# Kernel tuning notes

Measured on AMD Instinct MI355X. Metric: run time of the kernel, lower is better.

## Reference

```python
import jax, jax.numpy as jnp
import numpy as np


def setup_inputs() -> dict:
    key = jax.random.key(0)
    k1, k2, k3 = jax.random.split(key, 3)
    B, F, H, W = 16, 16, 256, 256
    inp = jax.random.normal(k1, (B, F, H, W), dtype=jnp.float32)
    target = jax.random.normal(k2, (B, F, H, W), dtype=jnp.float32)
    masks = jax.random.randint(k3, (B, F, H, W), 0, 2).astype(jnp.bool_)
    hull = jnp.zeros((1,), dtype=jnp.int32)  # unused by the module's forward
    return {"input": inp, "target": target, "masks": masks, "hull": hull}


def _masked_mean_per_feature(diff, w):
    # diff: [B,F,H,W]; w: float mask broadcastable to diff. Returns [F] masked means
    # with 0.0 where the mask is empty (matching the torch `if len(diff) > 0` guard).
    s = jnp.sum(diff * w, axis=(0, 2, 3))                               # [F]
    c = jnp.sum(jnp.broadcast_to(w, diff.shape), axis=(0, 2, 3))        # [F]
    return jnp.where(c > 0, s / jnp.maximum(c, 1.0), 0.0)


def reference(input, target, masks, hull):
    diff = jnp.abs(input - target)                                      # [B,F,H,W]
    m = masks.astype(diff.dtype)                                        # feature masks
    m_not = 1.0 - m                                                     # background
    m_all = jnp.any(masks, axis=1, keepdims=True).astype(diff.dtype)    # [B,1,H,W]

    loss_features = jnp.mean(_masked_mean_per_feature(diff, m))
    loss_background = jnp.mean(_masked_mean_per_feature(diff, m_not))
    loss_all_features = jnp.mean(_masked_mean_per_feature(diff, m_all))

    return (loss_features + loss_all_features + loss_background) / 3.0
```

## Files before the change

kernel.cpp:

```cpp
#include <hip/hip_runtime.h>

constexpr int B = 16, F = 16, H = 256, W = 256;
constexpr int HW = H * W;
constexpr int SPATIAL = B * HW;
constexpr int PLANE4 = HW / 4;
constexpr int BSTRIDE4 = F * PLANE4;
constexpr int FQ = 4;

constexpr int NBLK = 2048;
constexpr int NTHREADS = 256;
constexpr int NWAVES = NTHREADS / 64;
constexpr int TOTG = B * PLANE4;
constexpr int SLOTS = NBLK * NWAVES * 16;
constexpr int G = TOTG / SLOTS;
static_assert(G == 2, "kernel below is hand-scheduled for G==2");

constexpr int NVALS = 50;

struct Buf {
    unsigned int m[FQ];
    float4 a[FQ];
    float4 t[FQ];
};

__global__ __launch_bounds__(NTHREADS) void heatloss_main(
        const float4* __restrict__ inp, const float4* __restrict__ tgt,
        const unsigned int* __restrict__ msk, float* __restrict__ partials) {
    const int tid  = threadIdx.x;
    const int wave = tid >> 6;
    const int lane = tid & 63;
    const int l16  = lane & 15;
    const int q    = lane >> 4;
    const int slot0 = (blockIdx.x * NWAVES + wave) * 16 + l16;
    const int qoff  = q * (FQ * PLANE4);

    float s[FQ]  = {0.f, 0.f, 0.f, 0.f};
    float c[FQ]  = {0.f, 0.f, 0.f, 0.f};
    float dt[FQ] = {0.f, 0.f, 0.f, 0.f};
    float sall = 0.f, call = 0.f;

    auto load_group = [&](Buf& bf, int it) {
        const int slot = slot0 + it * SLOTS;
        const int base = (slot >> 14) * BSTRIDE4 + (slot & (PLANE4 - 1)) + qoff;
        #pragma unroll
        for (int j = 0; j < FQ; j++) bf.m[j] = msk[base + j * PLANE4];
        #pragma unroll
        for (int j = 0; j < FQ; j++) bf.a[j] = inp[base + j * PLANE4];
        #pragma unroll
        for (int j = 0; j < FQ; j++) bf.t[j] = tgt[base + j * PLANE4];
    };

    auto consume = [&](const Buf& bf) {
        unsigned int anyu = bf.m[0] | bf.m[1] | bf.m[2] | bf.m[3];
        anyu |= __shfl_xor(anyu, 16, 64);
        anyu |= __shfl_xor(anyu, 32, 64);
        const float af0 = (anyu & 0x000000FFu) ? 1.f : 0.f;
        const float af1 = (anyu & 0x0000FF00u) ? 1.f : 0.f;
        const float af2 = (anyu & 0x00FF0000u) ? 1.f : 0.f;
        const float af3 = (anyu & 0xFF000000u) ? 1.f : 0.f;
        if (q == 0) call += (af0 + af1) + (af2 + af3);

        #pragma unroll
        for (int j = 0; j < FQ; j++) {
            const float4 a = bf.a[j];
            const float4 t = bf.t[j];
            const float d0 = fabsf(a.x - t.x);
            const float d1 = fabsf(a.y - t.y);
            const float d2 = fabsf(a.z - t.z);
            const float d3 = fabsf(a.w - t.w);
            const unsigned int mm = bf.m[j];
            const float m0 = (float)( mm        & 0xFFu);
            const float m1 = (float)((mm >> 8)  & 0xFFu);
            const float m2 = (float)((mm >> 16) & 0xFFu);
            const float m3 = (float)( mm >> 24);
            dt[j] += (d0 + d1) + (d2 + d3);
            s[j]  += m0 * d0 + m1 * d1 + m2 * d2 + m3 * d3;
            c[j]  += (m0 + m1) + (m2 + m3);
            sall  += af0 * d0 + af1 * d1 + af2 * d2 + af3 * d3;
        }
    };

    Buf b0, b1;
    load_group(b0, 0);
    load_group(b1, 1);
    asm volatile("" ::: "memory");
    consume(b0);
    consume(b1);

    __shared__ float red[NWAVES][NVALS];
    const int fbase = q * FQ;
    #pragma unroll
    for (int j = 0; j < FQ; j++) {
        float xs = s[j], xc = c[j], xd = dt[j];
        #pragma unroll
        for (int o = 8; o > 0; o >>= 1) {
            xs += __shfl_down(xs, o, 16);
            xc += __shfl_down(xc, o, 16);
            xd += __shfl_down(xd, o, 16);
        }
        if (l16 == 0) {
            red[wave][ 0 + fbase + j] = xs;
            red[wave][16 + fbase + j] = xc;
            red[wave][32 + fbase + j] = xd;
        }
    }
    float xa = sall, xcl = call;
    #pragma unroll
    for (int o = 32; o > 0; o >>= 1) {
        xa  += __shfl_down(xa,  o, 64);
        xcl += __shfl_down(xcl, o, 64);
    }
    if (lane == 0) { red[wave][48] = xa; red[wave][49] = xcl; }
    __syncthreads();

    if (tid < NVALS) {
        float t = 0.f;
        #pragma unroll
        for (int w2 = 0; w2 < NWAVES; w2++) t += red[w2][tid];
        partials[tid * NBLK + blockIdx.x] = t;
    }
}

__global__ __launch_bounds__(NTHREADS) void heatloss_final(
        const float* __restrict__ partials, float* __restrict__ out) {
    const int tid  = threadIdx.x;
    const int wave = tid >> 6;
    const int lane = tid & 63;
    __shared__ float vals[NVALS];
    for (int v = wave; v < NVALS; v += NWAVES) {
        const float* p = partials + v * NBLK;
        float x = 0.f;
        #pragma unroll
        for (int k = 0; k < NBLK / 64; k++) x += p[lane + k * 64];
        #pragma unroll
        for (int o = 32; o > 0; o >>= 1) x += __shfl_down(x, o, 64);
        if (lane == 0) vals[v] = x;
    }
    __syncthreads();
    if (tid == 0) {
        const float Nf = (float)SPATIAL;
        float lf = 0.f, lbg = 0.f;
        #pragma unroll
        for (int f = 0; f < F; f++) {
            const float sf = vals[f], cf = vals[16 + f], dtf = vals[32 + f];
            lf += (cf > 0.f) ? sf / cf : 0.f;
            const float sbg = dtf - sf, cbg = Nf - cf;
            lbg += (cbg > 0.f) ? sbg / cbg : 0.f;
        }
        const float sa = vals[48], cl = vals[49];
        const float lall = (cl > 0.f) ? sa / cl : 0.f;
        out[0] = (lf / 16.f + lbg / 16.f + lall / 16.f) / 3.f;
    }
}

extern "C" void kernel_launch(void* const* d_in, const int* in_sizes, int n_in,
                              void* d_out, int out_size, void* d_ws, size_t ws_size,
                              hipStream_t stream) {
    const float4*       inp = (const float4*)d_in[0];
    const float4*       tgt = (const float4*)d_in[1];
    const unsigned int* msk = (const unsigned int*)d_in[2];
    float* out      = (float*)d_out;
    float* partials = (float*)d_ws;

    heatloss_main<<<NBLK, NTHREADS, 0, stream>>>(inp, tgt, msk, partials);
    heatloss_final<<<1, NTHREADS, 0, stream>>>(partials, out);
}
```

Baseline: 197.0 us.

## Remap threads so each wave owns four features across 64 contiguous pixels

Instead of splitting a wave into four 16-lane quarters that each cover four features, every wave now handles four features for 64 consecutive float4 pixels. Each wave's loads become 1 KB contiguous segments per feature plane rather than 256-byte pieces. The cross-feature OR for the any-mask now goes through shared memory with a __syncthreads per iteration instead of wave shuffles, which adds block-level synchronisation between load and compute. Loads for the second group are no longer issued before the first group is consumed, so less memory latency is hidden.

```diff
diff --git a/kernel.cpp b/kernel.cpp
--- a/kernel.cpp
+++ b/kernel.cpp
@@ -5,23 +5,15 @@
 constexpr int SPATIAL = B * HW;
 constexpr int PLANE4 = HW / 4;
 constexpr int BSTRIDE4 = F * PLANE4;
-constexpr int FQ = 4;
 
 constexpr int NBLK = 2048;
 constexpr int NTHREADS = 256;
 constexpr int NWAVES = NTHREADS / 64;
-constexpr int TOTG = B * PLANE4;
-constexpr int SLOTS = NBLK * NWAVES * 16;
-constexpr int G = TOTG / SLOTS;
-static_assert(G == 2, "kernel below is hand-scheduled for G==2");
+constexpr int G = 2;
+constexpr int TOT4 = B * PLANE4;
+static_assert(NBLK * G * 64 == TOT4, "coverage must be exact");
 
 constexpr int NVALS = 50;
-
-struct Buf {
-    unsigned int m[FQ];
-    float4 a[FQ];
-    float4 t[FQ];
-};
 
 __global__ __launch_bounds__(NTHREADS) void heatloss_main(
         const float4* __restrict__ inp, const float4* __restrict__ tgt,
@@ -29,46 +21,53 @@
     const int tid  = threadIdx.x;
     const int wave = tid >> 6;
     const int lane = tid & 63;
-    const int l16  = lane & 15;
-    const int q    = lane >> 4;
-    const int slot0 = (blockIdx.x * NWAVES + wave) * 16 + l16;
-    const int qoff  = q * (FQ * PLANE4);
+    const int foff = (wave * 4) * PLANE4;
 
-    float s[FQ]  = {0.f, 0.f, 0.f, 0.f};
-    float c[FQ]  = {0.f, 0.f, 0.f, 0.f};
-    float dt[FQ] = {0.f, 0.f, 0.f, 0.f};
+    float s[4]  = {0.f, 0.f, 0.f, 0.f};
+    float c[4]  = {0.f, 0.f, 0.f, 0.f};
+    float dt[4] = {0.f, 0.f, 0.f, 0.f};
     float sall = 0.f, call = 0.f;
 
-    auto load_group = [&](Buf& bf, int it) {
-        const int slot = slot0 + it * SLOTS;
-        const int base = (slot >> 14) * BSTRIDE4 + (slot & (PLANE4 - 1)) + qoff;
+    __shared__ unsigned int anybuf[2][NWAVES][64];
+
+    #pragma unroll
+    for (int it = 0; it < G; ++it) {
+        const int slot = blockIdx.x * G + it;
+        const int gidx = slot * 64 + lane;
+        const int b    = gidx >> 14;
+        const int hw4  = gidx & (PLANE4 - 1);
+        const int base = b * BSTRIDE4 + foff + hw4;
+
+        unsigned int m[4];
+        float4 av[4], tv[4];
         #pragma unroll
-        for (int j = 0; j < FQ; j++) bf.m[j] = msk[base + j * PLANE4];
+        for (int j = 0; j < 4; j++) m[j] = msk[base + j * PLANE4];
         #pragma unroll
-        for (int j = 0; j < FQ; j++) bf.a[j] = inp[base + j * PLANE4];
+        for (int j = 0; j < 4; j++) av[j] = inp[base + j * PLANE4];
         #pragma unroll
-        for (int j = 0; j < FQ; j++) bf.t[j] = tgt[base + j * PLANE4];
-    };
+        for (int j = 0; j < 4; j++) tv[j] = tgt[base + j * PLANE4];
 
-    auto consume = [&](const Buf& bf) {
-        unsigned int anyu = bf.m[0] | bf.m[1] | bf.m[2] | bf.m[3];
-        anyu |= __shfl_xor(anyu, 16, 64);
-        anyu |= __shfl_xor(anyu, 32, 64);
-        const float af0 = (anyu & 0x000000FFu) ? 1.f : 0.f;
-        const float af1 = (anyu & 0x0000FF00u) ? 1.f : 0.f;
-        const float af2 = (anyu & 0x00FF0000u) ? 1.f : 0.f;
-        const float af3 = (anyu & 0xFF000000u) ? 1.f : 0.f;
-        if (q == 0) call += (af0 + af1) + (af2 + af3);
+        const unsigned int anyw = m[0] | m[1] | m[2] | m[3];
+        anybuf[it & 1][wave][lane] = anyw;
+        __syncthreads();
+        const unsigned int any = anybuf[it & 1][0][lane] | anybuf[it & 1][1][lane]
+                               | anybuf[it & 1][2][lane] | anybuf[it & 1][3][lane];
+
+        const float af0 = (any & 0x000000FFu) ? 1.f : 0.f;
+        const float af1 = (any & 0x0000FF00u) ? 1.f : 0.f;
+        const float af2 = (any & 0x00FF0000u) ? 1.f : 0.f;
+        const float af3 = (any & 0xFF000000u) ? 1.f : 0.f;
+        if (wave == 0) call += (af0 + af1) + (af2 + af3);
 
         #pragma unroll
-        for (int j = 0; j < FQ; j++) {
-            const float4 a = bf.a[j];
-            const float4 t = bf.t[j];
+        for (int j = 0; j < 4; j++) {
+            const float4 a = av[j];
+            const float4 t = tv[j];
             const float d0 = fabsf(a.x - t.x);
             const float d1 = fabsf(a.y - t.y);
             const float d2 = fabsf(a.z - t.z);
             const float d3 = fabsf(a.w - t.w);
-            const unsigned int mm = bf.m[j];
+            const unsigned int mm = m[j];
             const float m0 = (float)( mm        & 0xFFu);
             const float m1 = (float)((mm >> 8)  & 0xFFu);
             const float m2 = (float)((mm >> 16) & 0xFFu);
@@ -78,30 +77,22 @@
             c[j]  += (m0 + m1) + (m2 + m3);
             sall  += af0 * d0 + af1 * d1 + af2 * d2 + af3 * d3;
         }
-    };
+    }
 
-    Buf b0, b1;
-    load_group(b0, 0);
-    load_group(b1, 1);
-    asm volatile("" ::: "memory");
-    consume(b0);
-    consume(b1);
-
-    __shared__ float red[NWAVES][NVALS];
-    const int fbase = q * FQ;
+    __shared__ float red[NWAVES][14];
     #pragma unroll
-    for (int j = 0; j < FQ; j++) {
+    for (int j = 0; j < 4; j++) {
         float xs = s[j], xc = c[j], xd = dt[j];
         #pragma unroll
-        for (int o = 8; o > 0; o >>= 1) {
-            xs += __shfl_down(xs, o, 16);
-            xc += __shfl_down(xc, o, 16);
-            xd += __shfl_down(xd, o, 16);
+        for (int o = 32; o > 0; o >>= 1) {
+            xs += __shfl_down(xs, o, 64);
+            xc += __shfl_down(xc, o, 64);
+            xd += __shfl_down(xd, o, 64);
         }
-        if (l16 == 0) {
-            red[wave][ 0 + fbase + j] = xs;
-            red[wave][16 + fbase + j] = xc;
-            red[wave][32 + fbase + j] = xd;
+        if (lane == 0) {
+            red[wave][0 + j] = xs;
+            red[wave][4 + j] = xc;
+            red[wave][8 + j] = xd;
         }
     }
     float xa = sall, xcl = call;
@@ -110,13 +101,24 @@
         xa  += __shfl_down(xa,  o, 64);
         xcl += __shfl_down(xcl, o, 64);
     }
-    if (lane == 0) { red[wave][48] = xa; red[wave][49] = xcl; }
+    if (lane == 0) { red[wave][12] = xa; red[wave][13] = xcl; }
     __syncthreads();
 
     if (tid < NVALS) {
-        float t = 0.f;
-        #pragma unroll
-        for (int w2 = 0; w2 < NWAVES; w2++) t += red[w2][tid];
+        float t;
+        if (tid < 16) {
+            t = red[tid >> 2][0 + (tid & 3)];
+        } else if (tid < 32) {
+            const int f = tid - 16;
+            t = red[f >> 2][4 + (f & 3)];
+        } else if (tid < 48) {
+            const int f = tid - 32;
+            t = red[f >> 2][8 + (f & 3)];
+        } else if (tid == 48) {
+            t = (red[0][12] + red[1][12]) + (red[2][12] + red[3][12]);
+        } else {
+            t = (red[0][13] + red[1][13]) + (red[2][13] + red[3][13]);
+        }
         partials[tid * NBLK + blockIdx.x] = t;
     }
 }
```

New measurement: 192.1 us. 2.5% less time.
